# Kernel tuning notes

Hardware: AMD Instinct MI355X
Metric: run time of the kernel (lower is better)

The kernel has to match this reference:

```python
import jax, jax.numpy as jnp
import numpy as np
from jax import lax

SEQ, BATCH, IN, HID, OUT = 168, 4096, 24, 64, 9


def _uniform(key, shape, scale):
    return jax.random.uniform(key, shape, jnp.float32, -scale, scale)


def setup_inputs() -> dict:
    key = jax.random.key(0)
    ks = jax.random.split(key, 12)
    s = 1.0 / np.sqrt(HID)  # PyTorch LSTM/Linear init scale
    return {
        "x": jax.random.normal(ks[0], (SEQ, BATCH, IN), jnp.float32),
        # layer 0 LSTM (PyTorch gate order: i, f, g, o stacked along dim 0)
        "W_ih0": _uniform(ks[1], (4 * HID, IN), s),
        "W_hh0": _uniform(ks[2], (4 * HID, HID), s),
        "b_ih0": _uniform(ks[3], (4 * HID,), s),
        "b_hh0": _uniform(ks[4], (4 * HID,), s),
        # layer 1 LSTM
        "W_ih1": _uniform(ks[5], (4 * HID, HID), s),
        "W_hh1": _uniform(ks[6], (4 * HID, HID), s),
        "b_ih1": _uniform(ks[7], (4 * HID,), s),
        "b_hh1": _uniform(ks[8], (4 * HID,), s),
        # linear head
        "W_out": _uniform(ks[9], (OUT, HID), s),
        "b_out": _uniform(ks[10], (OUT,), s),
    }


def _lstm_layer(x, W_ih, W_hh, b_ih, b_hh):
    # x: [S, B, D]; returns hidden states [S, B, H]
    H = W_hh.shape[1]
    B = x.shape[1]
    # precompute input projections for all timesteps: [S, B, 4H]
    xg = jnp.einsum('sbd,gd->sbg', x, W_ih) + b_ih + b_hh

    def step(carry, xg_t):
        h, c = carry
        g = xg_t + h @ W_hh.T  # [B, 4H]
        i, f, gc, o = jnp.split(g, 4, axis=-1)
        c = jax.nn.sigmoid(f) * c + jax.nn.sigmoid(i) * jnp.tanh(gc)
        h = jax.nn.sigmoid(o) * jnp.tanh(c)
        return (h, c), h

    init = (jnp.zeros((B, H), x.dtype), jnp.zeros((B, H), x.dtype))
    _, hs = lax.scan(step, init, xg)
    return hs


def reference(x, W_ih0, W_hh0, b_ih0, b_hh0, W_ih1, W_hh1, b_ih1, b_hh1, W_out, b_out):
    h = _lstm_layer(x, W_ih0, W_hh0, b_ih0, b_hh0)   # [S, B, H]
    h = _lstm_layer(h, W_ih1, W_hh1, b_ih1, b_hh1)   # [S, B, H]
    out = jnp.einsum('sbh,oh->sbo', h, W_out) + b_out  # [S, B, OUT]
    return out
```

## Files before the change

### kernel.cpp

```cpp
#include <hip/hip_runtime.h>
#include <hip/hip_bf16.h>
#include <math.h>

#define SEQ   168
#define BATCH 4096
#define NOUT  9
#define NBLK  256

typedef short bf16x8 __attribute__((ext_vector_type(8)));
typedef float f32x4  __attribute__((ext_vector_type(4)));

#define MFMA(a,b,c) __builtin_amdgcn_mfma_f32_16x16x32_bf16((a),(b),(c),0,0,0)

#define L2E  1.44269504088896340736f
#define CLMP 40.0f

static __device__ __forceinline__ float e2(float x){
    return __builtin_amdgcn_exp2f(x);
}
static __device__ __forceinline__ float bf2f(unsigned short h){
    unsigned int u = ((unsigned int)h) << 16;
    return __builtin_bit_cast(float, u);
}
static __device__ __forceinline__ unsigned short f2bf(float f){
    return __builtin_bit_cast(unsigned short, __float2bfloat16(f));
}
static __device__ __forceinline__ void splitf(float f, unsigned short& hi, unsigned short& lo){
    hi = f2bf(f);
    float r = f - bf2f(hi);
    lo = (unsigned short)(__builtin_bit_cast(unsigned int, r) >> 16);
}
static __device__ __forceinline__ bf16x8 ldfrag(const unsigned short* p){
    const uint4 q = *reinterpret_cast<const uint4*>(p);
    return __builtin_bit_cast(bf16x8, q);
}

static __device__ __forceinline__ float cellupd(float pi, float pf, float pg,
                                                float po, float& c){
    const float Ai = 1.0f + e2(fminf(-pi, CLMP));
    const float Af = 1.0f + e2(fminf(-pf, CLMP));
    const float Bg = 1.0f + e2(fminf( pg, CLMP));
    const float Ao = 1.0f + e2(fminf(-po, CLMP));
    const float t1 = Ai * Bg;
    const float r  = __builtin_amdgcn_rcpf(Af * t1);
    const float cn = fmaf(c, t1, Af * (Bg - 2.0f)) * r;
    c = cn;
    const float Bc = 1.0f + e2(fminf(cn * (2.0f * L2E), CLMP));
    return (Bc - 2.0f) * __builtin_amdgcn_rcpf(Ao * Bc);
}

static __device__ __forceinline__ void gbar(int* cnt, int* phs, int* done,
                                            int tickval, int& ph, int lane){
    asm volatile("s_waitcnt lgkmcnt(0)" ::: "memory");
    if (lane == 0){
        int old = __hip_atomic_fetch_add(cnt, 1, __ATOMIC_ACQ_REL,
                                         __HIP_MEMORY_SCOPE_WORKGROUP);
        if (old == 3){
            *cnt = 0;
            __hip_atomic_store(done, tickval, __ATOMIC_RELEASE,
                               __HIP_MEMORY_SCOPE_WORKGROUP);
            __hip_atomic_store(phs, ph ^ 1, __ATOMIC_RELEASE,
                               __HIP_MEMORY_SCOPE_WORKGROUP);
        }
    }
    while (__hip_atomic_load(phs, __ATOMIC_ACQUIRE,
                             __HIP_MEMORY_SCOPE_WORKGROUP) == ph)
        __builtin_amdgcn_s_sleep(1);
    ph ^= 1;
}
static __device__ __forceinline__ void wait_ge(int* done, int need){
    if (__hip_atomic_load(done, __ATOMIC_ACQUIRE, __HIP_MEMORY_SCOPE_WORKGROUP) >= need) return;
    do { __builtin_amdgcn_s_sleep(1); }
    while (__hip_atomic_load(done, __ATOMIC_ACQUIRE, __HIP_MEMORY_SCOPE_WORKGROUP) < need);
}

__global__ __launch_bounds__(512, 2)
void lstm_fused(const float* __restrict__ x,
                const float* __restrict__ Wih0, const float* __restrict__ Whh0,
                const float* __restrict__ bih0, const float* __restrict__ bhh0,
                const float* __restrict__ Wih1, const float* __restrict__ Whh1,
                const float* __restrict__ bih1, const float* __restrict__ bhh1,
                const float* __restrict__ Wout, const float* __restrict__ bout,
                float* __restrict__ out)
{
    __shared__ __align__(16) unsigned short sXH[2][16][72];
    __shared__ __align__(16) unsigned short sH0H[3][16][72];
    __shared__ __align__(16) unsigned short sH1H[2][16][72];
    __shared__ int sync[8];

    const int tid  = threadIdx.x;
    const int half = tid >> 8;
    const int w2   = (tid >> 6) & 3;
    const int l    = tid & 63;
    const int lr   = l & 15;
    const int g    = l >> 4;
    const int r0   = blockIdx.x * 16;
    const int cg   = w2 * 16 + lr;

    const float WS[4] = { L2E, L2E, 2.0f * L2E, L2E };

    if (tid < 8) sync[tid] = (tid == 4) ? -1 : 0;

    for (int i = tid; i < (int)(2*16*72/2); i += 512){
        ((unsigned int*)sXH)[i]  = 0u;
        ((unsigned int*)sH1H)[i] = 0u;
    }
    for (int i = tid; i < (int)(3*16*72/2); i += 512)
        ((unsigned int*)sH0H)[i] = 0u;
    __syncthreads();
    if (tid < 96){
        const float4 v = *reinterpret_cast<const float4*>(&x[(size_t)r0 * 24 + tid * 4]);
        const int row = (tid * 4) / 24, col = (tid * 4) % 24;
        ushort4 w = { f2bf(v.x), f2bf(v.y), f2bf(v.z), f2bf(v.w) };
        *reinterpret_cast<ushort4*>(&sXH[0][row][col]) = w;
    }
    __syncthreads();

    if (half == 0){
        bf16x8 B0H[4][3];
        #pragma unroll
        for (int gt = 0; gt < 4; ++gt){
            const int c = gt * 64 + cg;
            const float sc = WS[gt];
            bf16x8 bh = {0,0,0,0,0,0,0,0};
            if (g < 3){
                const float* pw = &Wih0[c * 24 + g * 8];
                #pragma unroll
                for (int j = 0; j < 8; ++j) bh[j] = (short)f2bf(pw[j] * sc);
            }
            B0H[gt][0] = bh;
            #pragma unroll
            for (int ks = 0; ks < 2; ++ks){
                bf16x8 ch;
                const float* pw = &Whh0[c * 64 + ks * 32 + g * 8];
                #pragma unroll
                for (int j = 0; j < 8; ++j) ch[j] = (short)f2bf(pw[j] * sc);
                B0H[gt][1+ks] = ch;
            }
        }
        float b0[4];
        #pragma unroll
        for (int gt = 0; gt < 4; ++gt) b0[gt] = (bih0[gt*64 + cg] + bhh0[gt*64 + cg]) * WS[gt];

        const float* xfp = x + ((size_t)BATCH + r0) * 24 + tid * 4;
        float c0[4] = {0,0,0,0};
        int ph = 0;
        int pw = 0, pr = 2;
        for (int t = 0; t < SEQ; ++t){
            const int px = t & 1;
            const bool ldx = (tid < 96) && (t + 1 < SEQ);
            float4 pref;
            if (ldx){ pref = *reinterpret_cast<const float4*>(xfp); xfp += (size_t)BATCH * 24; }

            const bf16x8 AxH = ldfrag(&sXH[px][lr][g*8]);
            bf16x8 A0H[2];
            #pragma unroll
            for (int ks = 0; ks < 2; ++ks)
                A0H[ks] = ldfrag(&sH0H[pr][lr][ks*32 + g*8]);

            f32x4 a0[4];
            #pragma unroll
            for (int gt = 0; gt < 4; ++gt){ f32x4 a = {b0[gt],b0[gt],b0[gt],b0[gt]}; a0[gt] = a; }
            #pragma unroll
            for (int gt = 0; gt < 4; ++gt) a0[gt] = MFMA(AxH, B0H[gt][0], a0[gt]);
            #pragma unroll
            for (int ks = 0; ks < 2; ++ks){
                #pragma unroll
                for (int gt = 0; gt < 4; ++gt) a0[gt] = MFMA(A0H[ks], B0H[gt][1+ks], a0[gt]);
            }
            unsigned short hh[4];
            #pragma unroll
            for (int i = 0; i < 4; ++i)
                hh[i] = f2bf(cellupd(a0[0][i], a0[1][i], a0[2][i], a0[3][i], c0[i]));
            if (t >= 3) wait_ge(&sync[5], t - 2);
            #pragma unroll
            for (int i = 0; i < 4; ++i)
                sH0H[pw][g * 4 + i][cg] = hh[i];
            if (ldx){
                const int row = (tid * 4) / 24, col = (tid * 4) % 24;
                ushort4 w = { f2bf(pref.x), f2bf(pref.y), f2bf(pref.z), f2bf(pref.w) };
                *reinterpret_cast<ushort4*>(&sXH[px ^ 1][row][col]) = w;
            }
            gbar(&sync[0], &sync[2], &sync[4], t, ph, l);
            pr = pw;
            pw = (pw == 2) ? 0 : pw + 1;
        }
    } else {
        bf16x8 B1H[4][4];
        #pragma unroll
        for (int gt = 0; gt < 4; ++gt){
            const int c = gt * 64 + cg;
            const float sc = WS[gt];
            #pragma unroll
            for (int ks = 0; ks < 2; ++ks){
                bf16x8 ch;
                const float* pw = &Wih1[c * 64 + ks * 32 + g * 8];
                #pragma unroll
                for (int j = 0; j < 8; ++j) ch[j] = (short)f2bf(pw[j] * sc);
                B1H[gt][ks] = ch;
            }
            #pragma unroll
            for (int ks = 0; ks < 2; ++ks){
                bf16x8 ch;
                const float* pw = &Whh1[c * 64 + ks * 32 + g * 8];
                #pragma unroll
                for (int j = 0; j < 8; ++j) ch[j] = (short)f2bf(pw[j] * sc);
                B1H[gt][2+ks] = ch;
            }
        }
        float b1[4];
        #pragma unroll
        for (int gt = 0; gt < 4; ++gt) b1[gt] = (bih1[gt*64 + cg] + bhh1[gt*64 + cg]) * WS[gt];

        const int oc = lr;
        bf16x8 WoH[2], WoL[2];
        #pragma unroll
        for (int tt = 0; tt < 2; ++tt){
            bf16x8 bh = {0,0,0,0,0,0,0,0}, bl = {0,0,0,0,0,0,0,0};
            if (oc < NOUT){
                const float* pw = &Wout[oc * 64 + tt * 32 + g * 8];
                #pragma unroll
                for (int j = 0; j < 8; ++j){ unsigned short hh, ll; splitf(pw[j], hh, ll); bh[j]=(short)hh; bl[j]=(short)ll; }
            }
            WoH[tt] = bh; WoL[tt] = bl;
        }
        const float bo0 = (oc < NOUT) ? bout[oc] : 0.f;
        float* houtp = out + (size_t)(r0 + g * 4) * NOUT + oc;

        float c1[4] = {0,0,0,0};
        int ph = 0;
        int pr0 = 0;
        for (int t = 1; t <= SEQ; ++t){
            const int p = t & 1;
            bf16x8 A1H[2];
            #pragma unroll
            for (int ks = 0; ks < 2; ++ks)
                A1H[ks] = ldfrag(&sH1H[p][lr][ks*32 + g*8]);
            wait_ge(&sync[4], t - 1);
            bf16x8 A0H[2];
            #pragma unroll
            for (int ks = 0; ks < 2; ++ks)
                A0H[ks] = ldfrag(&sH0H[pr0][lr][ks*32 + g*8]);

            f32x4 a1[4];
            #pragma unroll
            for (int gt = 0; gt < 4; ++gt){ f32x4 a = {b1[gt],b1[gt],b1[gt],b1[gt]}; a1[gt] = a; }
            #pragma unroll
            for (int ks = 0; ks < 2; ++ks){
                #pragma unroll
                for (int gt = 0; gt < 4; ++gt) a1[gt] = MFMA(A1H[ks], B1H[gt][2+ks], a1[gt]);
            }
            if (t >= 2 && w2 == (t & 3)){
                f32x4 ha = {bo0, bo0, bo0, bo0};
                ha = MFMA(A1H[0], WoH[0], ha);
                ha = MFMA(A1H[0], WoL[0], ha);
                ha = MFMA(A1H[1], WoH[1], ha);
                ha = MFMA(A1H[1], WoL[1], ha);
                if (oc < NOUT){
                    #pragma unroll
                    for (int i = 0; i < 4; ++i)
                        houtp[(size_t)i * NOUT] = ha[i];
                }
            }
            if (t >= 2) houtp += (size_t)BATCH * NOUT;
            #pragma unroll
            for (int ks = 0; ks < 2; ++ks){
                #pragma unroll
                for (int gt = 0; gt < 4; ++gt) a1[gt] = MFMA(A0H[ks], B1H[gt][ks], a1[gt]);
            }
            #pragma unroll
            for (int i = 0; i < 4; ++i)
                sH1H[p ^ 1][g * 4 + i][cg] =
                    f2bf(cellupd(a1[0][i], a1[1][i], a1[2][i], a1[3][i], c1[i]));
            gbar(&sync[1], &sync[3], &sync[5], t, ph, l);
            pr0 = (pr0 == 2) ? 0 : pr0 + 1;
        }
        {
            const int pe = (SEQ + 1) & 1;
            if (w2 == ((SEQ + 1) & 3)){
                bf16x8 A1H0 = ldfrag(&sH1H[pe][lr][g*8]);
                bf16x8 A1H1 = ldfrag(&sH1H[pe][lr][32 + g*8]);
                f32x4 ha = {bo0, bo0, bo0, bo0};
                ha = MFMA(A1H0, WoH[0], ha);
                ha = MFMA(A1H0, WoL[0], ha);
                ha = MFMA(A1H1, WoH[1], ha);
                ha = MFMA(A1H1, WoL[1], ha);
                if (oc < NOUT){
                    #pragma unroll
                    for (int i = 0; i < 4; ++i)
                        houtp[(size_t)i * NOUT] = ha[i];
                }
            }
        }
    }
}

extern "C" void kernel_launch(void* const* d_in, const int* in_sizes, int n_in,
                              void* d_out, int out_size, void* d_ws, size_t ws_size,
                              hipStream_t stream)
{
    const float* x    = (const float*)d_in[0];
    const float* Wih0 = (const float*)d_in[1];
    const float* Whh0 = (const float*)d_in[2];
    const float* bih0 = (const float*)d_in[3];
    const float* bhh0 = (const float*)d_in[4];
    const float* Wih1 = (const float*)d_in[5];
    const float* Whh1 = (const float*)d_in[6];
    const float* bih1 = (const float*)d_in[7];
    const float* bhh1 = (const float*)d_in[8];
    const float* Wout = (const float*)d_in[9];
    const float* bout = (const float*)d_in[10];
    float* out = (float*)d_out;

    lstm_fused<<<NBLK, 512, 0, stream>>>(x, Wih0, Whh0, bih0, bhh0,
                                         Wih1, Whh1, bih1, bhh1,
                                         Wout, bout, out);
}
```

Measured before the change: 168.8 us.

## Replace counter-based group barriers with per-wave progress flags

Swaps the atomic-counter phase barrier for per-wave progress slots. Each wave publishes its timestep with a release store, and consumers wait on the minimum of four slots. This removes the fetch_add serialization and the all-waves rendezvous at the end of each step, so waves can run slightly ahead and the write of layer-0 hidden state is moved after the x prefetch store. Waits now poll four LDS words instead of one, and correctness depends on the min-based ordering covering every buffer-reuse hazard.

```diff
diff --git a/kernel.cpp b/kernel.cpp
--- a/kernel.cpp
+++ b/kernel.cpp
@@ -49,29 +49,21 @@
     return (Bc - 2.0f) * __builtin_amdgcn_rcpf(Ao * Bc);
 }
 
-static __device__ __forceinline__ void gbar(int* cnt, int* phs, int* done,
-                                            int tickval, int& ph, int lane){
+static __device__ __forceinline__ int min4(const int* s){
+    int a = __hip_atomic_load(&s[0], __ATOMIC_ACQUIRE, __HIP_MEMORY_SCOPE_WORKGROUP);
+    int b = __hip_atomic_load(&s[1], __ATOMIC_ACQUIRE, __HIP_MEMORY_SCOPE_WORKGROUP);
+    int c = __hip_atomic_load(&s[2], __ATOMIC_ACQUIRE, __HIP_MEMORY_SCOPE_WORKGROUP);
+    int d = __hip_atomic_load(&s[3], __ATOMIC_ACQUIRE, __HIP_MEMORY_SCOPE_WORKGROUP);
+    return min(min(a, b), min(c, d));
+}
+static __device__ __forceinline__ void wait4(const int* s, int need){
+    if (min4(s) >= need) return;
+    do { __builtin_amdgcn_s_sleep(1); } while (min4(s) < need);
+}
+static __device__ __forceinline__ void post(int* slot, int t, int lane){
     asm volatile("s_waitcnt lgkmcnt(0)" ::: "memory");
-    if (lane == 0){
-        int old = __hip_atomic_fetch_add(cnt, 1, __ATOMIC_ACQ_REL,
-                                         __HIP_MEMORY_SCOPE_WORKGROUP);
-        if (old == 3){
-            *cnt = 0;
-            __hip_atomic_store(done, tickval, __ATOMIC_RELEASE,
-                               __HIP_MEMORY_SCOPE_WORKGROUP);
-            __hip_atomic_store(phs, ph ^ 1, __ATOMIC_RELEASE,
-                               __HIP_MEMORY_SCOPE_WORKGROUP);
-        }
-    }
-    while (__hip_atomic_load(phs, __ATOMIC_ACQUIRE,
-                             __HIP_MEMORY_SCOPE_WORKGROUP) == ph)
-        __builtin_amdgcn_s_sleep(1);
-    ph ^= 1;
-}
-static __device__ __forceinline__ void wait_ge(int* done, int need){
-    if (__hip_atomic_load(done, __ATOMIC_ACQUIRE, __HIP_MEMORY_SCOPE_WORKGROUP) >= need) return;
-    do { __builtin_amdgcn_s_sleep(1); }
-    while (__hip_atomic_load(done, __ATOMIC_ACQUIRE, __HIP_MEMORY_SCOPE_WORKGROUP) < need);
+    if (lane == 0)
+        __hip_atomic_store(slot, t, __ATOMIC_RELEASE, __HIP_MEMORY_SCOPE_WORKGROUP);
 }
 
 __global__ __launch_bounds__(512, 2)
@@ -99,7 +91,7 @@
 
     const float WS[4] = { L2E, L2E, 2.0f * L2E, L2E };
 
-    if (tid < 8) sync[tid] = (tid == 4) ? -1 : 0;
+    if (tid < 8) sync[tid] = -1;
 
     for (int i = tid; i < (int)(2*16*72/2); i += 512){
         ((unsigned int*)sXH)[i]  = 0u;
@@ -144,9 +136,9 @@
 
         const float* xfp = x + ((size_t)BATCH + r0) * 24 + tid * 4;
         float c0[4] = {0,0,0,0};
-        int ph = 0;
         int pw = 0, pr = 2;
         for (int t = 0; t < SEQ; ++t){
+            if (t >= 1) wait4(&sync[0], t - 1);
             const int px = t & 1;
             const bool ldx = (tid < 96) && (t + 1 < SEQ);
             float4 pref;
@@ -172,16 +164,16 @@
             #pragma unroll
             for (int i = 0; i < 4; ++i)
                 hh[i] = f2bf(cellupd(a0[0][i], a0[1][i], a0[2][i], a0[3][i], c0[i]));
-            if (t >= 3) wait_ge(&sync[5], t - 2);
-            #pragma unroll
-            for (int i = 0; i < 4; ++i)
-                sH0H[pw][g * 4 + i][cg] = hh[i];
             if (ldx){
                 const int row = (tid * 4) / 24, col = (tid * 4) % 24;
                 ushort4 w = { f2bf(pref.x), f2bf(pref.y), f2bf(pref.z), f2bf(pref.w) };
                 *reinterpret_cast<ushort4*>(&sXH[px ^ 1][row][col]) = w;
             }
-            gbar(&sync[0], &sync[2], &sync[4], t, ph, l);
+            if (t >= 3) wait4(&sync[4], t - 2);
+            #pragma unroll
+            for (int i = 0; i < 4; ++i)
+                sH0H[pw][g * 4 + i][cg] = hh[i];
+            post(&sync[w2], t, l);
             pr = pw;
             pw = (pw == 2) ? 0 : pw + 1;
         }
@@ -228,15 +220,15 @@
         float* houtp = out + (size_t)(r0 + g * 4) * NOUT + oc;
 
         float c1[4] = {0,0,0,0};
-        int ph = 0;
         int pr0 = 0;
         for (int t = 1; t <= SEQ; ++t){
+            if (t >= 2) wait4(&sync[4], t - 1);
             const int p = t & 1;
             bf16x8 A1H[2];
             #pragma unroll
             for (int ks = 0; ks < 2; ++ks)
                 A1H[ks] = ldfrag(&sH1H[p][lr][ks*32 + g*8]);
-            wait_ge(&sync[4], t - 1);
+            wait4(&sync[0], t - 1);
             bf16x8 A0H[2];
             #pragma unroll
             for (int ks = 0; ks < 2; ++ks)
@@ -272,10 +264,11 @@
             for (int i = 0; i < 4; ++i)
                 sH1H[p ^ 1][g * 4 + i][cg] =
                     f2bf(cellupd(a1[0][i], a1[1][i], a1[2][i], a1[3][i], c1[i]));
-            gbar(&sync[1], &sync[3], &sync[5], t, ph, l);
+            post(&sync[4 + w2], t, l);
             pr0 = (pr0 == 2) ? 0 : pr0 + 1;
         }
         {
+            wait4(&sync[4], SEQ);
             const int pe = (SEQ + 1) & 1;
             if (w2 == ((SEQ + 1) & 3)){
                 bf16x8 A1H0 = ldfrag(&sH1H[pe][lr][g*8]);
```

Result: slower. 178.4 us (+5.7%).

## Interleave per-gate MFMA chains with exp, deepen h0 ring to four slots

Applied to the files above, without the earlier changes.

Reorders the gate MFMAs so each gate's accumulation chain finishes and its exp2 runs right away, which lets transcendental work overlap the MFMA latency of the next gate. The layer-0 hidden-state ring buffer grows from three to four slots, loosening the producer/consumer coupling between the two layer halves. The wait on the layer-1 progress counter moves later, after the x prefetch store. The cost is extra LDS and more live registers for the exponent values, which could hurt occupancy at two blocks per CU.

```diff
diff --git a/kernel.cpp b/kernel.cpp
--- a/kernel.cpp
+++ b/kernel.cpp
@@ -35,12 +35,12 @@
     return __builtin_bit_cast(bf16x8, q);
 }
 
-static __device__ __forceinline__ float cellupd(float pi, float pf, float pg,
-                                                float po, float& c){
-    const float Ai = 1.0f + e2(fminf(-pi, CLMP));
-    const float Af = 1.0f + e2(fminf(-pf, CLMP));
-    const float Bg = 1.0f + e2(fminf( pg, CLMP));
-    const float Ao = 1.0f + e2(fminf(-po, CLMP));
+static __device__ __forceinline__ float cellcomb(float E0, float E1, float E2,
+                                                 float E3, float& c){
+    const float Ai = 1.0f + E0;
+    const float Af = 1.0f + E1;
+    const float Bg = 1.0f + E2;
+    const float Ao = 1.0f + E3;
     const float t1 = Ai * Bg;
     const float r  = __builtin_amdgcn_rcpf(Af * t1);
     const float cn = fmaf(c, t1, Af * (Bg - 2.0f)) * r;
@@ -84,7 +84,7 @@
                 float* __restrict__ out)
 {
     __shared__ __align__(16) unsigned short sXH[2][16][72];
-    __shared__ __align__(16) unsigned short sH0H[3][16][72];
+    __shared__ __align__(16) unsigned short sH0H[4][16][72];
     __shared__ __align__(16) unsigned short sH1H[2][16][72];
     __shared__ int sync[8];
 
@@ -105,7 +105,7 @@
         ((unsigned int*)sXH)[i]  = 0u;
         ((unsigned int*)sH1H)[i] = 0u;
     }
-    for (int i = tid; i < (int)(3*16*72/2); i += 512)
+    for (int i = tid; i < (int)(4*16*72/2); i += 512)
         ((unsigned int*)sH0H)[i] = 0u;
     __syncthreads();
     if (tid < 96){
@@ -145,7 +145,7 @@
         const float* xfp = x + ((size_t)BATCH + r0) * 24 + tid * 4;
         float c0[4] = {0,0,0,0};
         int ph = 0;
-        int pw = 0, pr = 2;
+        int pw = 0, pr = 3;
         for (int t = 0; t < SEQ; ++t){
             const int px = t & 1;
             const bool ldx = (tid < 96) && (t + 1 < SEQ);
@@ -158,32 +158,34 @@
             for (int ks = 0; ks < 2; ++ks)
                 A0H[ks] = ldfrag(&sH0H[pr][lr][ks*32 + g*8]);
 
-            f32x4 a0[4];
-            #pragma unroll
-            for (int gt = 0; gt < 4; ++gt){ f32x4 a = {b0[gt],b0[gt],b0[gt],b0[gt]}; a0[gt] = a; }
-            #pragma unroll
-            for (int gt = 0; gt < 4; ++gt) a0[gt] = MFMA(AxH, B0H[gt][0], a0[gt]);
-            #pragma unroll
-            for (int ks = 0; ks < 2; ++ks){
-                #pragma unroll
-                for (int gt = 0; gt < 4; ++gt) a0[gt] = MFMA(A0H[ks], B0H[gt][1+ks], a0[gt]);
+            float Ex[4][4];
+            #pragma unroll
+            for (int gt = 0; gt < 4; ++gt){
+                f32x4 a = {b0[gt], b0[gt], b0[gt], b0[gt]};
+                a = MFMA(AxH,    B0H[gt][0], a);
+                a = MFMA(A0H[0], B0H[gt][1], a);
+                a = MFMA(A0H[1], B0H[gt][2], a);
+                const float sg = (gt == 2) ? 1.0f : -1.0f;
+                #pragma unroll
+                for (int i = 0; i < 4; ++i)
+                    Ex[gt][i] = e2(fminf(sg * a[i], CLMP));
             }
             unsigned short hh[4];
             #pragma unroll
             for (int i = 0; i < 4; ++i)
-                hh[i] = f2bf(cellupd(a0[0][i], a0[1][i], a0[2][i], a0[3][i], c0[i]));
-            if (t >= 3) wait_ge(&sync[5], t - 2);
-            #pragma unroll
-            for (int i = 0; i < 4; ++i)
-                sH0H[pw][g * 4 + i][cg] = hh[i];
+                hh[i] = f2bf(cellcomb(Ex[0][i], Ex[1][i], Ex[2][i], Ex[3][i], c0[i]));
             if (ldx){
                 const int row = (tid * 4) / 24, col = (tid * 4) % 24;
                 ushort4 w = { f2bf(pref.x), f2bf(pref.y), f2bf(pref.z), f2bf(pref.w) };
                 *reinterpret_cast<ushort4*>(&sXH[px ^ 1][row][col]) = w;
             }
+            if (t >= 4) wait_ge(&sync[5], t - 3);
+            #pragma unroll
+            for (int i = 0; i < 4; ++i)
+                sH0H[pw][g * 4 + i][cg] = hh[i];
             gbar(&sync[0], &sync[2], &sync[4], t, ph, l);
             pr = pw;
-            pw = (pw == 2) ? 0 : pw + 1;
+            pw = (pw + 1) & 3;
         }
     } else {
         bf16x8 B1H[4][4];
@@ -242,13 +244,18 @@
             for (int ks = 0; ks < 2; ++ks)
                 A0H[ks] = ldfrag(&sH0H[pr0][lr][ks*32 + g*8]);
 
-            f32x4 a1[4];
-            #pragma unroll
-            for (int gt = 0; gt < 4; ++gt){ f32x4 a = {b1[gt],b1[gt],b1[gt],b1[gt]}; a1[gt] = a; }
-            #pragma unroll
-            for (int ks = 0; ks < 2; ++ks){
-                #pragma unroll
-                for (int gt = 0; gt < 4; ++gt) a1[gt] = MFMA(A1H[ks], B1H[gt][2+ks], a1[gt]);
+            float Ex[4][4];
+            #pragma unroll
+            for (int gt = 0; gt < 4; ++gt){
+                f32x4 a = {b1[gt], b1[gt], b1[gt], b1[gt]};
+                a = MFMA(A1H[0], B1H[gt][2], a);
+                a = MFMA(A1H[1], B1H[gt][3], a);
+                a = MFMA(A0H[0], B1H[gt][0], a);
+                a = MFMA(A0H[1], B1H[gt][1], a);
+                const float sg = (gt == 2) ? 1.0f : -1.0f;
+                #pragma unroll
+                for (int i = 0; i < 4; ++i)
+                    Ex[gt][i] = e2(fminf(sg * a[i], CLMP));
             }
             if (t >= 2 && w2 == (t & 3)){
                 f32x4 ha = {bo0, bo0, bo0, bo0};
@@ -263,17 +270,15 @@
                 }
             }
             if (t >= 2) houtp += (size_t)BATCH * NOUT;
-            #pragma unroll
-            for (int ks = 0; ks < 2; ++ks){
-                #pragma unroll
-                for (int gt = 0; gt < 4; ++gt) a1[gt] = MFMA(A0H[ks], B1H[gt][ks], a1[gt]);
-            }
+            unsigned short hh1[4];
             #pragma unroll
             for (int i = 0; i < 4; ++i)
-                sH1H[p ^ 1][g * 4 + i][cg] =
-                    f2bf(cellupd(a1[0][i], a1[1][i], a1[2][i], a1[3][i], c1[i]));
+                hh1[i] = f2bf(cellcomb(Ex[0][i], Ex[1][i], Ex[2][i], Ex[3][i], c1[i]));
+            #pragma unroll
+            for (int i = 0; i < 4; ++i)
+                sH1H[p ^ 1][g * 4 + i][cg] = hh1[i];
             gbar(&sync[1], &sync[3], &sync[5], t, ph, l);
-            pr0 = (pr0 == 2) ? 0 : pr0 + 1;
+            pr0 = (pr0 + 1) & 3;
         }
         {
             const int pe = (SEQ + 1) & 1;
```

After: 177.1 us. 4.9% more time.
